# Kernel tuning notes

Hardware: AMD Instinct MI355X
Metric: run time of the kernel (lower is better)

The kernel has to match this reference:

```python
import jax, jax.numpy as jnp
import numpy as np

B_, T_, D_MODEL = 2, 2048, 1024
EXPAND, D_STATE, D_CONV, HEADDIM = 2, 128, 4, 64
D_INNER = EXPAND * D_MODEL            # 2048
NHEADS = D_INNER // HEADDIM           # 32
CONV_DIM = D_INNER + 2 * D_STATE      # 2304 (x, B, C share the depthwise conv)
D_IN_PROJ = 2 * D_INNER + 2 * D_STATE + NHEADS  # z, xBC, dt


def _rmsnorm(x, w, eps=1e-5):
    return x * jax.lax.rsqrt(jnp.mean(x * x, axis=-1, keepdims=True) + eps) * w


def setup_inputs() -> dict:
    key = jax.random.key(0)
    ks = jax.random.split(key, 8)
    def s(k, shape, scale=0.02):
        return jax.random.normal(k, shape, jnp.float32) * scale
    x = jax.random.normal(ks[0], (B_, T_, D_MODEL), jnp.float32)
    W_in = s(ks[1], (D_MODEL, D_IN_PROJ))
    conv_w = s(ks[2], (CONV_DIM, D_CONV), 0.1)
    conv_b = jnp.zeros((CONV_DIM,), jnp.float32)
    # dt_bias = softplus^-1(dt_init) with dt in [1e-3, 1e-1], per Mamba init
    dt0 = jax.random.uniform(ks[3], (NHEADS,), minval=1e-3, maxval=1e-1)
    dt_bias = jnp.log(jnp.expm1(dt0))
    A_log = jnp.log(jax.random.uniform(ks[4], (NHEADS,), minval=1.0, maxval=16.0))
    D = jnp.ones((NHEADS,), jnp.float32)
    norm_w = jnp.ones((D_MODEL,), jnp.float32)
    gnorm_w = jnp.ones((D_INNER,), jnp.float32)
    W_out = s(ks[5], (D_INNER, D_MODEL))
    return {"x": x, "W_in": W_in, "conv_w": conv_w, "conv_b": conv_b,
            "dt_bias": dt_bias, "A_log": A_log, "D": D,
            "norm_w": norm_w, "gnorm_w": gnorm_w, "W_out": W_out}


def reference(x, W_in, conv_w, conv_b, dt_bias, A_log, D, norm_w, gnorm_w, W_out):
    res = x
    xn = _rmsnorm(x, norm_w)                       # pre-norm
    zxbcdt = xn @ W_in                             # (B,T,D_IN_PROJ)
    z = zxbcdt[..., :D_INNER]
    xBC = zxbcdt[..., D_INNER:D_INNER + CONV_DIM]
    dt = zxbcdt[..., D_INNER + CONV_DIM:]          # (B,T,H)
    # causal depthwise conv over time on concat(x,B,C)
    inp = jnp.transpose(xBC, (0, 2, 1))            # (B,C,T)
    kern = conv_w[:, None, :]                      # (C,1,K)
    conv = jax.lax.conv_general_dilated(
        inp, kern, window_strides=(1,), padding=[(D_CONV - 1, 0)],
        feature_group_count=CONV_DIM, dimension_numbers=("NCH", "OIH", "NCH"))
    xBC = jax.nn.silu(jnp.transpose(conv, (0, 2, 1)) + conv_b)
    xs = xBC[..., :D_INNER].reshape(B_, T_, NHEADS, HEADDIM)  # (B,T,H,P)
    Bm = xBC[..., D_INNER:D_INNER + D_STATE]       # (B,T,N), ngroups=1
    C = xBC[..., D_INNER + D_STATE:]               # (B,T,N)
    dt = jax.nn.softplus(dt + dt_bias)             # (B,T,H)
    A = -jnp.exp(A_log)                            # (H,)

    def step(h, inps):
        x_t, B_t, C_t, dt_t = inps                 # (B,H,P),(B,N),(B,N),(B,H)
        da = jnp.exp(dt_t * A)                     # (B,H)
        h = h * da[:, :, None, None] + (dt_t[..., None] * x_t)[..., None] * B_t[:, None, None, :]
        y = jnp.einsum("bhpn,bn->bhp", h, C_t) + D[None, :, None] * x_t
        return h, y

    h0 = jnp.zeros((B_, NHEADS, HEADDIM, D_STATE), x.dtype)
    seq = (jnp.moveaxis(xs, 1, 0), jnp.moveaxis(Bm, 1, 0),
           jnp.moveaxis(C, 1, 0), jnp.moveaxis(dt, 1, 0))
    _, ys = jax.lax.scan(step, h0, seq)            # ys: (T,B,H,P)
    y = jnp.moveaxis(ys, 0, 1).reshape(B_, T_, D_INNER)
    y = _rmsnorm(y * jax.nn.silu(z), gnorm_w)      # gated RMSNorm
    return y @ W_out + res
```

## Files before the change

### kernel.cpp

```cpp
#include <hip/hip_runtime.h>
#include <hip/hip_bf16.h>

typedef unsigned short u16;
typedef unsigned int u32;
typedef u16 u16x8 __attribute__((ext_vector_type(8)));
typedef u16 u16x4 __attribute__((ext_vector_type(4)));
typedef __bf16 bf16x8 __attribute__((ext_vector_type(8)));
typedef float f32x4 __attribute__((ext_vector_type(4)));

#define B_SZ 2
#define T_SZ 2048
#define DMODEL 1024
#define DINNER 2048
#define DSTATE 128
#define NHEADS 32
#define HEADDIM 64
#define CONVDIM 2304
#define DINPROJ 4384
#define DINPROJ_P 4480
#define NROWS (B_SZ * T_SZ)
#define L_CH 128
#define NCH 16

__device__ __forceinline__ float bf2f(u16 u) {
    union { float f; u32 i; } v; v.i = ((u32)u) << 16; return v.f;
}
__device__ __forceinline__ u16 f2bf(float f) {
    union { float f; u32 i; } v; v.f = f;
    u32 r = v.i + 0x7FFFu + ((v.i >> 16) & 1u);
    return (u16)(r >> 16);
}
__device__ __forceinline__ bf16x8 ldfrag(const u16* p) {
    return __builtin_bit_cast(bf16x8, *(const u16x8*)p);
}
__device__ __forceinline__ void gload_lds16(const u16* g, u16* l) {
    __builtin_amdgcn_global_load_lds(
        (const __attribute__((address_space(1))) unsigned int*)g,
        (__attribute__((address_space(3))) unsigned int*)l, 16, 0, 0);
}

__device__ void trans_tile(const float* __restrict__ in, u16* __restrict__ out,
                           int K, int N, int n0, int k0)
{
    __shared__ u16 tile[64][72];
    const int tid = threadIdx.x;
#pragma unroll
    for (int r = 0; r < 4; r++) {
        int idx = r * 256 + tid;
        int k = idx >> 4, n4 = (idx & 15) << 2;
        const float* src = &in[(size_t)(k0 + k) * N + n0 + n4];
        float4 v;
        if (n0 + n4 + 3 < N) {
            v = *(const float4*)src;
        } else {
            v.x = (n0 + n4 + 0 < N) ? src[0] : 0.f;
            v.y = (n0 + n4 + 1 < N) ? src[1] : 0.f;
            v.z = (n0 + n4 + 2 < N) ? src[2] : 0.f;
            v.w = (n0 + n4 + 3 < N) ? src[3] : 0.f;
        }
        tile[n4 + 0][k] = f2bf(v.x);
        tile[n4 + 1][k] = f2bf(v.y);
        tile[n4 + 2][k] = f2bf(v.z);
        tile[n4 + 3][k] = f2bf(v.w);
    }
    __syncthreads();
#pragma unroll
    for (int r = 0; r < 2; r++) {
        int idx = r * 256 + tid;
        int n = idx >> 3, k8 = (idx & 7) << 3;
        u16x8 vv = *(const u16x8*)&tile[n][k8];
        *(u16x8*)&out[(size_t)(n0 + n) * K + k0 + k8] = vv;
    }
}

__global__ __launch_bounds__(256) void prep_kernel(
    const float* __restrict__ W_in, u16* __restrict__ W_inT,
    const float* __restrict__ W_out, u16* __restrict__ W_outT,
    const float* __restrict__ x, const float* __restrict__ nw, u16* __restrict__ xn,
    const float* __restrict__ cw, u16* __restrict__ cwT)
{
    const int blk = blockIdx.x;
    const int tid = threadIdx.x;
    if (blk < 1120) {
        trans_tile(W_in, W_inT, DMODEL, DINPROJ, (blk % 70) * 64, (blk / 70) * 64);
    } else if (blk < 1632) {
        int idx = blk - 1120;
        trans_tile(W_out, W_outT, DINNER, DMODEL, (idx % 16) * 64, (idx / 16) * 64);
    } else if (blk < 5728) {
        const int row = blk - 1632;
        float4 v = ((const float4*)(x + (size_t)row * DMODEL))[tid];
        float ss = v.x * v.x + v.y * v.y + v.z * v.z + v.w * v.w;
#pragma unroll
        for (int o = 32; o; o >>= 1) ss += __shfl_xor(ss, o);
        __shared__ float red[4];
        if ((tid & 63) == 0) red[tid >> 6] = ss;
        __syncthreads();
        ss = red[0] + red[1] + red[2] + red[3];
        float sc = rsqrtf(ss / (float)DMODEL + 1e-5f);
        float4 wv = ((const float4*)nw)[tid];
        u16x4 o4;
        o4[0] = f2bf(v.x * sc * wv.x);
        o4[1] = f2bf(v.y * sc * wv.y);
        o4[2] = f2bf(v.z * sc * wv.z);
        o4[3] = f2bf(v.w * sc * wv.w);
        *(u16x4*)&xn[(size_t)row * DMODEL + tid * 4] = o4;
    } else {
        for (int idx = tid; idx < 4 * CONVDIM; idx += 256) {
            int k = idx / CONVDIM, c = idx - k * CONVDIM;
            cwT[idx] = f2bf(cw[c * 4 + k]);
        }
    }
}

template<int MODE, int KC, int SWZ>
__global__ __launch_bounds__(256) void gemm128_kernel(
    const u16* __restrict__ A, const u16* __restrict__ BT, void* __restrict__ Cv,
    const float* __restrict__ Res, int Nst, int nbx)
{
    __shared__ u16 As[128 * 64];
    __shared__ u16 Bs[128 * 64];
    const int tid = threadIdx.x;
    const int l = tid & 63, w = tid >> 6;
    int m0, n0;
    if (SWZ) {
        const int bid = blockIdx.x;
        int s = (bid & 7) * 140 + (bid >> 3);
        int mc = s / 280, r2 = s - mc * 280;
        int nc = (r2 >= 144) ? 1 : 0;
        int local = r2 - nc * 144;
        int nloc = local >> 3, mloc = local & 7;
        m0 = (mc * 8 + mloc) * 128;
        n0 = (nc * 18 + nloc) * 128;
    } else {
        const int per = nbx * 8;
        const int grp = blockIdx.x / per, r = blockIdx.x % per;
        m0 = (grp * 8 + (r & 7)) * 128;
        n0 = (r >> 3) * 128;
    }
    const int ml = l & 15, quad = l >> 4;
    const int wm = (w & 1) * 64, wn = (w >> 1) * 64;
    f32x4 acc[4][4] = {};
    const int srow = l >> 3;
    const int sgx = (l & 7) ^ srow;
    const u16* Ag = A + (size_t)(m0 + w * 8 + srow) * KC + sgx * 8;
    const u16* Bg = BT + (size_t)(n0 + w * 8 + srow) * KC + sgx * 8;
    u16* const As_w = &As[(w * 8) * 64];
    u16* const Bs_w = &Bs[(w * 8) * 64];

#pragma unroll 4
    for (int k0 = 0; k0 < KC; k0 += 64) {
        __syncthreads();
#pragma unroll
        for (int j = 0; j < 4; j++) {
            gload_lds16(Ag + (size_t)(j * 32) * KC + k0, As_w + j * 32 * 64);
            gload_lds16(Bg + (size_t)(j * 32) * KC + k0, Bs_w + j * 32 * 64);
        }
        __syncthreads();
#pragma unroll
        for (int ks4 = 0; ks4 < 2; ks4++) {
            bf16x8 af[4], bfr[4];
#pragma unroll
            for (int i = 0; i < 4; i++)
                af[i] = ldfrag(&As[(wm + i * 16 + ml) * 64 +
                                   (((ks4 * 4 + quad) ^ (ml & 7)) * 8)]);
#pragma unroll
            for (int i = 0; i < 4; i++)
                bfr[i] = ldfrag(&Bs[(wn + i * 16 + ml) * 64 +
                                    (((ks4 * 4 + quad) ^ (ml & 7)) * 8)]);
#pragma unroll
            for (int mt = 0; mt < 4; mt++)
#pragma unroll
                for (int nt = 0; nt < 4; nt++)
                    acc[mt][nt] = __builtin_amdgcn_mfma_f32_16x16x32_bf16(
                        af[mt], bfr[nt], acc[mt][nt], 0, 0, 0);
        }
    }
#pragma unroll
    for (int mt = 0; mt < 4; mt++)
#pragma unroll
        for (int nt = 0; nt < 4; nt++)
#pragma unroll
            for (int rg = 0; rg < 4; rg++) {
                int m = m0 + wm + mt * 16 + quad * 4 + rg;
                int n = n0 + wn + nt * 16 + ml;
                if (n < Nst) {
                    if (MODE == 0)
                        ((u16*)Cv)[(size_t)m * Nst + n] = f2bf(acc[mt][nt][rg]);
                    else
                        ((float*)Cv)[(size_t)m * Nst + n] =
                            acc[mt][nt][rg] + Res[(size_t)m * Nst + n];
                }
            }
}

template<int KC>
__global__ __launch_bounds__(256) void gemm128x64_kernel(
    const u16* __restrict__ A, const u16* __restrict__ BT, float* __restrict__ C,
    const float* __restrict__ Res, int Nst)
{
    __shared__ u16 As[128 * 64];
    __shared__ u16 Bs[64 * 64];
    const int tid = threadIdx.x;
    const int l = tid & 63, w = tid >> 6;
    const int bid = blockIdx.x;
    const int xcd = bid & 7, local = bid >> 3;
    const int mc = xcd >> 1, nc = xcd & 1;
    const int nloc = local & 7, mloc = local >> 3;
    const int m0 = (mc * 8 + mloc) * 128;
    const int n0 = (nc * 8 + nloc) * 64;
    const int ml = l & 15, quad = l >> 4;
    const int wm = w * 32;
    f32x4 acc[2][4] = {};
    const int srow = l >> 3;
    const int sgx = (l & 7) ^ srow;
    const u16* Ag = A + (size_t)(m0 + w * 8 + srow) * KC + sgx * 8;
    const u16* Bg = BT + (size_t)(n0 + w * 8 + srow) * KC + sgx * 8;
    u16* const As_w = &As[(w * 8) * 64];
    u16* const Bs_w = &Bs[(w * 8) * 64];

#pragma unroll 4
    for (int k0 = 0; k0 < KC; k0 += 64) {
        __syncthreads();
#pragma unroll
        for (int j = 0; j < 4; j++)
            gload_lds16(Ag + (size_t)(j * 32) * KC + k0, As_w + j * 32 * 64);
#pragma unroll
        for (int j = 0; j < 2; j++)
            gload_lds16(Bg + (size_t)(j * 32) * KC + k0, Bs_w + j * 32 * 64);
        __syncthreads();
#pragma unroll
        for (int ks4 = 0; ks4 < 2; ks4++) {
            bf16x8 af[2], bfr[4];
#pragma unroll
            for (int i = 0; i < 2; i++)
                af[i] = ldfrag(&As[(wm + i * 16 + ml) * 64 +
                                   (((ks4 * 4 + quad) ^ (ml & 7)) * 8)]);
#pragma unroll
            for (int i = 0; i < 4; i++)
                bfr[i] = ldfrag(&Bs[(i * 16 + ml) * 64 +
                                    (((ks4 * 4 + quad) ^ (ml & 7)) * 8)]);
#pragma unroll
            for (int mt = 0; mt < 2; mt++)
#pragma unroll
                for (int nt = 0; nt < 4; nt++)
                    acc[mt][nt] = __builtin_amdgcn_mfma_f32_16x16x32_bf16(
                        bfr[nt], af[mt], acc[mt][nt], 0, 0, 0);
        }
    }
#pragma unroll
    for (int mt = 0; mt < 2; mt++) {
        const int m = m0 + wm + mt * 16 + ml;
#pragma unroll
        for (int nt = 0; nt < 4; nt++) {
            const int nb = n0 + nt * 16 + quad * 4;
            float4 r = *(const float4*)&Res[(size_t)m * Nst + nb];
            float4 o;
            o.x = acc[mt][nt][0] + r.x;
            o.y = acc[mt][nt][1] + r.y;
            o.z = acc[mt][nt][2] + r.z;
            o.w = acc[mt][nt][3] + r.w;
            *(float4*)&C[(size_t)m * Nst + nb] = o;
        }
    }
}

#define NGRAN (CONVDIM / 8)
__global__ __launch_bounds__(256) void conv_silu_kernel(
    const u16* __restrict__ zx, const u16* __restrict__ cwT,
    const float* __restrict__ cb, const float* __restrict__ dt_bias,
    u16* __restrict__ out, float* __restrict__ dts)
{
    int idx = blockIdx.x * 256 + threadIdx.x;
    if (idx < B_SZ * NHEADS * T_SZ) {
        int t = idx & (T_SZ - 1);
        int bh = idx >> 11;
        int h = bh & 31, b = bh >> 5;
        float v = bf2f(zx[(size_t)(b * T_SZ + t) * DINPROJ + (DINNER + CONVDIM) + h]) + dt_bias[h];
        float sp = (v > 20.f) ? v : log1pf(expf(v));
        dts[((size_t)bh << 11) + t] = sp;
    }
    int gr = idx % NGRAN;
    int bt = idx / NGRAN;
    int t = bt & (T_SZ - 1);
    int c0 = gr * 8;
    float acc[8];
#pragma unroll
    for (int u = 0; u < 8; u++) acc[u] = cb[c0 + u];
    const u16* base = zx + (size_t)bt * DINPROJ + DINNER + c0;
#pragma unroll
    for (int k = 0; k < 4; k++) {
        int tt = t - 3 + k;
        if (tt >= 0) {
            u16x8 xv = *(const u16x8*)(base + (ptrdiff_t)(k - 3) * DINPROJ);
            u16x8 wv = *(const u16x8*)&cwT[k * CONVDIM + c0];
#pragma unroll
            for (int u = 0; u < 8; u++)
                acc[u] += bf2f(xv[u]) * bf2f(wv[u]);
        }
    }
    u16 res[8];
#pragma unroll
    for (int u = 0; u < 8; u++) {
        float s = acc[u] / (1.f + expf(-acc[u]));
        res[u] = f2bf(s);
    }
    *(u16x8*)&out[(size_t)bt * CONVDIM + c0] = *(u16x8*)res;
}

__global__ __launch_bounds__(256) void chunk_state_kernel(
    const u16* __restrict__ xbc, const float* __restrict__ dts_g,
    const float* __restrict__ A_log, float* __restrict__ cs_g, u16* __restrict__ S_bf)
{
    const int g = blockIdx.x;
    const int b = g >> 9, rem = g & 511, c = rem >> 5, h = rem & 31;
    const int tid = threadIdx.x;
    __shared__ float tmp[128], dt_l[128], d2e[128];
    __shared__ u16 Xw[64][136];
    __shared__ u16 BsT[128][136];
    const float A = -__expf(A_log[h]);
    if (tid < 128) {
        float d = dts_g[(((size_t)(b * 32 + h)) << 11) + (c << 7) + tid];
        dt_l[tid] = d; tmp[tid] = d * A;
    }
    __syncthreads();
    for (int off = 1; off < 128; off <<= 1) {
        float add = 0.f;
        if (tid < 128 && tid >= off) add = tmp[tid - off];
        __syncthreads();
        if (tid < 128) tmp[tid] += add;
        __syncthreads();
    }
    if (tid < 128) {
        float cs = tmp[tid];
        cs_g[(((size_t)(b * 32 + h)) << 11) + (c << 7) + tid] = cs;
        d2e[tid] = __expf(tmp[127] - cs) * dt_l[tid];
    }
    __syncthreads();
    const size_t rowbase = ((size_t)(b * T_SZ + c * L_CH)) * CONVDIM;
#pragma unroll
    for (int r = 0; r < 4; r++) {
        int v = tid + r * 256;
        int t = v >> 3, p0 = (v & 7) << 3;
        u16x8 xv = *(const u16x8*)&xbc[rowbase + (size_t)t * CONVDIM + h * 64 + p0];
        float s = d2e[t];
        const int tc = (t & 7) | (((t >> 3) ^ ((p0 >> 3) & 15)) << 3);
#pragma unroll
        for (int u = 0; u < 8; u++) Xw[p0 + u][tc] = f2bf(bf2f(xv[u]) * s);
    }
#pragma unroll
    for (int r = 0; r < 8; r++) {
        int v = tid + r * 256;
        int t = v >> 4, n0 = (v & 15) << 3;
        u16x8 bv = *(const u16x8*)&xbc[rowbase + (size_t)t * CONVDIM + DINNER + n0];
        const int tc = (t & 7) | (((t >> 3) ^ ((n0 >> 3) & 15)) << 3);
#pragma unroll
        for (int u = 0; u < 8; u++) BsT[n0 + u][tc] = bv[u];
    }
    __syncthreads();
    const int lane = tid & 63, wv = tid >> 6, ml = lane & 15, quad = lane >> 4;
    f32x4 acc[8] = {};
    const int arow = wv * 16 + ml;
    const int asw = (arow >> 3) & 15;
    for (int k0 = 0; k0 < 128; k0 += 32) {
        bf16x8 af = ldfrag(&Xw[arow][(((k0 >> 3) + quad) ^ asw) << 3]);
#pragma unroll
        for (int nt = 0; nt < 8; nt++) {
            const int brow = nt * 16 + ml;
            bf16x8 bf = ldfrag(&BsT[brow][(((k0 >> 3) + quad) ^ ((brow >> 3) & 15)) << 3]);
            acc[nt] = __builtin_amdgcn_mfma_f32_16x16x32_bf16(bf, af, acc[nt], 0, 0, 0);
        }
    }
    const size_t base = (size_t)g * 8192;
    const int p = wv * 16 + ml;
#pragma unroll
    for (int nt = 0; nt < 8; nt++) {
        const int nb = nt * 16 + quad * 4;
        u16x4 pk;
#pragma unroll
        for (int rg = 0; rg < 4; rg++) pk[rg] = f2bf(acc[nt][rg]);
        *(u16x4*)&S_bf[base + p * 128 + nb] = pk;
    }
}

__global__ __launch_bounds__(256) void state_pass_kernel(
    const float* __restrict__ cs_g, u16* __restrict__ S_bf)
{
    const int bh = blockIdx.x >> 3, b = bh >> 5, h = bh & 31;
    const int off = (blockIdx.x & 7) * 1024 + threadIdx.x * 4;
    const float* csb = cs_g + (((size_t)(b * 32 + h)) << 11);
    float H[4] = {0.f, 0.f, 0.f, 0.f};
    const size_t step = (size_t)32 * 8192;
    size_t slot = ((size_t)(b * NCH * 32 + h)) * 8192 + off;
    u16x4 tv = *(const u16x4*)&S_bf[slot];
    for (int c = 0; c < NCH; c++) {
        u16x4 tvn = tv;
        if (c + 1 < NCH) tvn = *(const u16x4*)&S_bf[slot + step];
        float decay = __expf(csb[(c << 7) + 127]);
        u16x4 hw;
#pragma unroll
        for (int i = 0; i < 4; i++) hw[i] = f2bf(H[i]);
        *(u16x4*)&S_bf[slot] = hw;
#pragma unroll
        for (int i = 0; i < 4; i++) H[i] = H[i] * decay + bf2f(tv[i]);
        tv = tvn; slot += step;
    }
}

__global__ __launch_bounds__(256) void chunk_out_kernel(
    const u16* __restrict__ xbc, const float* __restrict__ dts_g,
    const float* __restrict__ cs_g, const u16* __restrict__ H_bf,
    const float* __restrict__ Dv, u16* __restrict__ yraw)
{
    const int g = blockIdx.x;
    const int b = g >> 9, rem = g & 511, c = rem >> 5, h = rem & 31;
    const int tid = threadIdx.x;
    __shared__ u16 Xs[64][136];
    __shared__ u16 Gs[128][40];
    __shared__ u16 Hs[64 * 128];
    __shared__ u16 Bsh[128 * 128];
    __shared__ float cs_l[128], P_l[128], dt_l[128];
    const size_t rowbase = ((size_t)(b * T_SZ + c * L_CH)) * CONVDIM;
    const u16* Cg = xbc + rowbase + DINNER + 128;
    const u16* Bg = xbc + rowbase + DINNER;
    const u16* Hg = H_bf + (size_t)g * 8192;
#pragma unroll
    for (int r = 0; r < 4; r++) {
        int i = r * 256 + tid;
        int row = i >> 4, slot = i & 15;
        gload_lds16(Hg + row * 128 + ((slot ^ (row & 15)) << 3), &Hs[i * 8]);
    }
#pragma unroll
    for (int r = 0; r < 8; r++) {
        int i = r * 256 + tid;
        int row = i >> 4, slot = i & 15;
        gload_lds16(Bg + (size_t)row * CONVDIM + ((slot ^ (row & 15)) << 3), &Bsh[i * 8]);
    }
    if (tid < 128) {
        float cs = cs_g[(((size_t)(b * 32 + h)) << 11) + (c << 7) + tid];
        cs_l[tid] = cs; P_l[tid] = __expf(cs);
        dt_l[tid] = dts_g[(((size_t)(b * 32 + h)) << 11) + (c << 7) + tid];
    }
#pragma unroll
    for (int r = 0; r < 4; r++) {
        int v = tid + r * 256; int t = v >> 3, p0 = (v & 7) << 3;
        u16x8 xv = *(const u16x8*)&xbc[rowbase + (size_t)t * CONVDIM + h * 64 + p0];
        const int tc = (t & 7) | (((t >> 3) ^ ((p0 >> 3) & 15)) << 3);
#pragma unroll
        for (int u = 0; u < 8; u++) Xs[p0 + u][tc] = xv[u];
    }
    __syncthreads();
    const int lane = tid & 63, wv = tid >> 6, ml = lane & 15, quad = lane >> 4;
    const int trow = wv * 32;
    bf16x8 cf[2][4];
#pragma unroll
    for (int mt = 0; mt < 2; mt++)
#pragma unroll
        for (int kk = 0; kk < 4; kk++)
            cf[mt][kk] = ldfrag(Cg + (size_t)(trow + mt * 16 + ml) * CONVDIM + kk * 32 + quad * 8);
    f32x4 accY[2][4] = {};
#pragma unroll
    for (int kk = 0; kk < 4; kk++) {
        const int sw = (((kk << 2) + quad) ^ ml) << 3;
#pragma unroll
        for (int pt = 0; pt < 4; pt++) {
            bf16x8 bf = ldfrag(&Hs[(pt * 16 + ml) * 128 + sw]);
            accY[0][pt] = __builtin_amdgcn_mfma_f32_16x16x32_bf16(cf[0][kk], bf, accY[0][pt], 0, 0, 0);
            accY[1][pt] = __builtin_amdgcn_mfma_f32_16x16x32_bf16(cf[1][kk], bf, accY[1][pt], 0, 0, 0);
        }
    }
#pragma unroll
    for (int mt = 0; mt < 2; mt++) {
#pragma unroll
        for (int rg = 0; rg < 4; rg++) {
            float pp = P_l[trow + mt * 16 + quad * 4 + rg];
#pragma unroll
            for (int pt = 0; pt < 4; pt++) accY[mt][pt][rg] *= pp;
        }
    }
    for (int js = 0; js < 4; js++) {
        const int j0 = js * 32;
        f32x4 Ga[2][2] = {};
#pragma unroll
        for (int kk = 0; kk < 4; kk++) {
            const int sw = (((kk << 2) + quad) ^ ml) << 3;
            bf16x8 bf0 = ldfrag(&Bsh[(j0 + ml) * 128 + sw]);
            bf16x8 bf1 = ldfrag(&Bsh[(j0 + 16 + ml) * 128 + sw]);
            Ga[0][0] = __builtin_amdgcn_mfma_f32_16x16x32_bf16(cf[0][kk], bf0, Ga[0][0], 0, 0, 0);
            Ga[0][1] = __builtin_amdgcn_mfma_f32_16x16x32_bf16(cf[0][kk], bf1, Ga[0][1], 0, 0, 0);
            Ga[1][0] = __builtin_amdgcn_mfma_f32_16x16x32_bf16(cf[1][kk], bf0, Ga[1][0], 0, 0, 0);
            Ga[1][1] = __builtin_amdgcn_mfma_f32_16x16x32_bf16(cf[1][kk], bf1, Ga[1][1], 0, 0, 0);
        }
#pragma unroll
        for (int mt = 0; mt < 2; mt++) {
#pragma unroll
            for (int jt = 0; jt < 2; jt++) {
#pragma unroll
                for (int rg = 0; rg < 4; rg++) {
                    int t = trow + mt * 16 + quad * 4 + rg;
                    int j = j0 + jt * 16 + ml;
                    float val = 0.f;
                    if (t >= j) val = Ga[mt][jt][rg] * __expf(cs_l[t] - cs_l[j]) * dt_l[j];
                    Gs[t][jt * 16 + ml] = f2bf(val);
                }
            }
        }
#pragma unroll
        for (int mt = 0; mt < 2; mt++) {
            bf16x8 ag = ldfrag(&Gs[trow + mt * 16 + ml][quad * 8]);
#pragma unroll
            for (int pt = 0; pt < 4; pt++) {
                const int xrow = pt * 16 + ml;
                bf16x8 bx = ldfrag(&Xs[xrow][(((j0 >> 3) + quad) ^ ((xrow >> 3) & 15)) << 3]);
                accY[mt][pt] = __builtin_amdgcn_mfma_f32_16x16x32_bf16(ag, bx, accY[mt][pt], 0, 0, 0);
            }
        }
    }
    const float Dh = Dv[h];
    const size_t ybase = ((size_t)(b * T_SZ + c * L_CH)) * DINNER;
#pragma unroll
    for (int mt = 0; mt < 2; mt++) {
#pragma unroll
        for (int pt = 0; pt < 4; pt++) {
#pragma unroll
            for (int rg = 0; rg < 4; rg++) {
                int t = trow + mt * 16 + quad * 4 + rg;
                int p = pt * 16 + ml;
                const int tc = (t & 7) | (((t >> 3) ^ ((p >> 3) & 15)) << 3);
                float v = accY[mt][pt][rg] + Dh * bf2f(Xs[p][tc]);
                yraw[ybase + (size_t)t * DINNER + h * 64 + p] = f2bf(v);
            }
        }
    }
}

__global__ __launch_bounds__(256) void postnorm_kernel(
    const u16* __restrict__ yraw, const u16* __restrict__ zx,
    const float* __restrict__ gw, u16* __restrict__ out)
{
    const int row = blockIdx.x;
    const int tid = threadIdx.x;
    u16x8 yv = *(const u16x8*)(yraw + (size_t)row * DINNER + tid * 8);
    u16x8 zv = *(const u16x8*)(zx + (size_t)row * DINPROJ + tid * 8);
    float vals[8]; float ss = 0.f;
#pragma unroll
    for (int i = 0; i < 8; i++) {
        float y = bf2f(yv[i]);
        float z = bf2f(zv[i]);
        float s = z / (1.f + expf(-z));
        float t = y * s; vals[i] = t; ss += t * t;
    }
#pragma unroll
    for (int o = 32; o; o >>= 1) ss += __shfl_xor(ss, o);
    __shared__ float red[4];
    if ((tid & 63) == 0) red[tid >> 6] = ss;
    __syncthreads();
    ss = red[0] + red[1] + red[2] + red[3];
    float sc = rsqrtf(ss / (float)DINNER + 1e-5f);
    u16 o8[8];
#pragma unroll
    for (int i = 0; i < 8; i++) o8[i] = f2bf(vals[i] * sc * gw[tid * 8 + i]);
    *(u16x8*)(out + (size_t)row * DINNER + tid * 8) = *(u16x8*)o8;
}

extern "C" void kernel_launch(void* const* d_in, const int* in_sizes, int n_in,
                              void* d_out, int out_size, void* d_ws, size_t ws_size,
                              hipStream_t stream) {
    const float* x       = (const float*)d_in[0];
    const float* W_in    = (const float*)d_in[1];
    const float* conv_w  = (const float*)d_in[2];
    const float* conv_b  = (const float*)d_in[3];
    const float* dt_bias = (const float*)d_in[4];
    const float* A_log   = (const float*)d_in[5];
    const float* Dv      = (const float*)d_in[6];
    const float* norm_w  = (const float*)d_in[7];
    const float* gnorm_w = (const float*)d_in[8];
    const float* W_out   = (const float*)d_in[9];
    float* out = (float*)d_out;

    char* ws = (char*)d_ws;
    u16*   xn    = (u16*)(ws);
    u16*   W_inT = (u16*)(ws + 8388608);
    u16*   S_bf  = (u16*)(ws);
    float* cs_g  = (float*)(ws + 16777216);
    u16*   zx    = (u16*)(ws + 17563648);
    u16*   xbc   = (u16*)(ws + 53477376);
    float* dts   = (float*)(ws + 72351744);
    u16*   yraw  = (u16*)(ws + 72876032);
    u16*   cwT   = (u16*)(ws + 89653248);
    u16*   W_outT= (u16*)(ws + 89671680);
    u16*   ynorm = yraw;

    prep_kernel<<<5729, 256, 0, stream>>>(
        W_in, W_inT, W_out, W_outT, x, norm_w, xn, conv_w, cwT);
    gemm128_kernel<0, DMODEL, 1><<<(DINPROJ_P / 128) * (NROWS / 128), 256, 0, stream>>>(
        xn, W_inT, zx, nullptr, DINPROJ, DINPROJ_P / 128);
    conv_silu_kernel<<<(NROWS * NGRAN) / 256, 256, 0, stream>>>(
        zx, cwT, conv_b, dt_bias, xbc, dts);
    chunk_state_kernel<<<B_SZ * NCH * NHEADS, 256, 0, stream>>>(xbc, dts, A_log, cs_g, S_bf);
    state_pass_kernel<<<B_SZ * NHEADS * 8, 256, 0, stream>>>(cs_g, S_bf);
    chunk_out_kernel<<<B_SZ * NCH * NHEADS, 256, 0, stream>>>(xbc, dts, cs_g, S_bf, Dv, yraw);
    postnorm_kernel<<<NROWS, 256, 0, stream>>>(yraw, zx, gnorm_w, ynorm);
    gemm128x64_kernel<DINNER><<<512, 256, 0, stream>>>(
        ynorm, W_outT, out, x, DMODEL);
}
```

Baseline: 261.1 us.

## Reuse conv input rows over 4 timesteps, shuffle scan, transpose MFMA outputs for packed stores

The conv+SiLU kernel now has each thread produce four consecutive timesteps. It loads 7 input rows and the 4 weight vectors once into registers instead of re-reading overlapping rows, and the launch grid is cut by four. The chunk_state prefix sum over dt*A uses a wavefront __shfl_up scan plus one cross-wave add, replacing the log-step shared-memory scan and its many barriers. In chunk_out the MFMA A/B operands are swapped so each lane owns a timestep row. That lets the G-matrix and y outputs be written as packed 4-element stores instead of scattered 2-byte stores. The new conv path uses more registers and has a redundant load-guard block.

```diff
diff --git a/kernel.cpp b/kernel.cpp
--- a/kernel.cpp
+++ b/kernel.cpp
@@ -280,31 +280,48 @@
         dts[((size_t)bh << 11) + t] = sp;
     }
     int gr = idx % NGRAN;
-    int bt = idx / NGRAN;
-    int t = bt & (T_SZ - 1);
+    int q  = idx / NGRAN;
+    int bt0 = q * 4;
+    int t0 = bt0 & (T_SZ - 1);
     int c0 = gr * 8;
-    float acc[8];
-#pragma unroll
-    for (int u = 0; u < 8; u++) acc[u] = cb[c0 + u];
-    const u16* base = zx + (size_t)bt * DINPROJ + DINNER + c0;
-#pragma unroll
-    for (int k = 0; k < 4; k++) {
-        int tt = t - 3 + k;
-        if (tt >= 0) {
-            u16x8 xv = *(const u16x8*)(base + (ptrdiff_t)(k - 3) * DINPROJ);
-            u16x8 wv = *(const u16x8*)&cwT[k * CONVDIM + c0];
+    const u16* base = zx + (size_t)bt0 * DINPROJ + DINNER + c0;
+    u16x8 xr[7];
+#pragma unroll
+    for (int i = 0; i < 7; i++) {
+        int tt = t0 + i - 3;
+        if (tt >= 0 && i < 7 - 0) {
+            xr[i] = (tt >= 0) ? *(const u16x8*)(base + (ptrdiff_t)(i - 3) * DINPROJ)
+                              : u16x8{};
+        }
+        if (tt < 0) xr[i] = u16x8{};
+        else xr[i] = *(const u16x8*)(base + (ptrdiff_t)(i - 3) * DINPROJ);
+    }
+    u16x8 wv[4];
+#pragma unroll
+    for (int k = 0; k < 4; k++) wv[k] = *(const u16x8*)&cwT[k * CONVDIM + c0];
+    float bias[8];
+#pragma unroll
+    for (int u = 0; u < 8; u++) bias[u] = cb[c0 + u];
+#pragma unroll
+    for (int u4 = 0; u4 < 4; u4++) {
+        float acc[8];
+#pragma unroll
+        for (int u = 0; u < 8; u++) acc[u] = bias[u];
+#pragma unroll
+        for (int k = 0; k < 4; k++) {
+            u16x8 xv = xr[u4 + k];
 #pragma unroll
             for (int u = 0; u < 8; u++)
-                acc[u] += bf2f(xv[u]) * bf2f(wv[u]);
-        }
-    }
-    u16 res[8];
-#pragma unroll
-    for (int u = 0; u < 8; u++) {
-        float s = acc[u] / (1.f + expf(-acc[u]));
-        res[u] = f2bf(s);
-    }
-    *(u16x8*)&out[(size_t)bt * CONVDIM + c0] = *(u16x8*)res;
+                acc[u] += bf2f(xv[u]) * bf2f(wv[k][u]);
+        }
+        u16 res[8];
+#pragma unroll
+        for (int u = 0; u < 8; u++) {
+            float s = acc[u] / (1.f + expf(-acc[u]));
+            res[u] = f2bf(s);
+        }
+        *(u16x8*)&out[(size_t)(bt0 + u4) * CONVDIM + c0] = *(u16x8*)res;
+    }
 }
 
 __global__ __launch_bounds__(256) void chunk_state_kernel(
@@ -315,32 +332,38 @@
     const int b = g >> 9, rem = g & 511, c = rem >> 5, h = rem & 31;
     const int tid = threadIdx.x;
     __shared__ float tmp[128], dt_l[128], d2e[128];
+    __shared__ float wtot;
     __shared__ u16 Xw[64][136];
     __shared__ u16 BsT[128][136];
     const float A = -__expf(A_log[h]);
+    float v = 0.f;
     if (tid < 128) {
         float d = dts_g[(((size_t)(b * 32 + h)) << 11) + (c << 7) + tid];
-        dt_l[tid] = d; tmp[tid] = d * A;
+        dt_l[tid] = d;
+        v = d * A;
+#pragma unroll
+        for (int off = 1; off < 64; off <<= 1) {
+            float pv = __shfl_up(v, off, 64);
+            if ((tid & 63) >= off) v += pv;
+        }
+        if (tid == 63) wtot = v;
     }
     __syncthreads();
-    for (int off = 1; off < 128; off <<= 1) {
-        float add = 0.f;
-        if (tid < 128 && tid >= off) add = tmp[tid - off];
-        __syncthreads();
-        if (tid < 128) tmp[tid] += add;
-        __syncthreads();
-    }
     if (tid < 128) {
-        float cs = tmp[tid];
-        cs_g[(((size_t)(b * 32 + h)) << 11) + (c << 7) + tid] = cs;
-        d2e[tid] = __expf(tmp[127] - cs) * dt_l[tid];
+        if (tid >= 64) v += wtot;
+        tmp[tid] = v;
+        cs_g[(((size_t)(b * 32 + h)) << 11) + (c << 7) + tid] = v;
+    }
+    __syncthreads();
+    if (tid < 128) {
+        d2e[tid] = __expf(tmp[127] - v) * dt_l[tid];
     }
     __syncthreads();
     const size_t rowbase = ((size_t)(b * T_SZ + c * L_CH)) * CONVDIM;
 #pragma unroll
     for (int r = 0; r < 4; r++) {
-        int v = tid + r * 256;
-        int t = v >> 3, p0 = (v & 7) << 3;
+        int vv = tid + r * 256;
+        int t = vv >> 3, p0 = (vv & 7) << 3;
         u16x8 xv = *(const u16x8*)&xbc[rowbase + (size_t)t * CONVDIM + h * 64 + p0];
         float s = d2e[t];
         const int tc = (t & 7) | (((t >> 3) ^ ((p0 >> 3) & 15)) << 3);
@@ -349,8 +372,8 @@
     }
 #pragma unroll
     for (int r = 0; r < 8; r++) {
-        int v = tid + r * 256;
-        int t = v >> 4, n0 = (v & 15) << 3;
+        int vv = tid + r * 256;
+        int t = vv >> 4, n0 = (vv & 15) << 3;
         u16x8 bv = *(const u16x8*)&xbc[rowbase + (size_t)t * CONVDIM + DINNER + n0];
         const int tc = (t & 7) | (((t >> 3) ^ ((n0 >> 3) & 15)) << 3);
 #pragma unroll
@@ -464,18 +487,17 @@
 #pragma unroll
         for (int pt = 0; pt < 4; pt++) {
             bf16x8 bf = ldfrag(&Hs[(pt * 16 + ml) * 128 + sw]);
-            accY[0][pt] = __builtin_amdgcn_mfma_f32_16x16x32_bf16(cf[0][kk], bf, accY[0][pt], 0, 0, 0);
-            accY[1][pt] = __builtin_amdgcn_mfma_f32_16x16x32_bf16(cf[1][kk], bf, accY[1][pt], 0, 0, 0);
+            accY[0][pt] = __builtin_amdgcn_mfma_f32_16x16x32_bf16(bf, cf[0][kk], accY[0][pt], 0, 0, 0);
+            accY[1][pt] = __builtin_amdgcn_mfma_f32_16x16x32_bf16(bf, cf[1][kk], accY[1][pt], 0, 0, 0);
         }
     }
 #pragma unroll
     for (int mt = 0; mt < 2; mt++) {
-#pragma unroll
-        for (int rg = 0; rg < 4; rg++) {
-            float pp = P_l[trow + mt * 16 + quad * 4 + rg];
-#pragma unroll
-            for (int pt = 0; pt < 4; pt++) accY[mt][pt][rg] *= pp;
-        }
+        const float pp = P_l[trow + mt * 16 + ml];
+#pragma unroll
+        for (int pt = 0; pt < 4; pt++)
+#pragma unroll
+            for (int rg = 0; rg < 4; rg++) accY[mt][pt][rg] *= pp;
     }
     for (int js = 0; js < 4; js++) {
         const int j0 = js * 32;
@@ -485,23 +507,26 @@
             const int sw = (((kk << 2) + quad) ^ ml) << 3;
             bf16x8 bf0 = ldfrag(&Bsh[(j0 + ml) * 128 + sw]);
             bf16x8 bf1 = ldfrag(&Bsh[(j0 + 16 + ml) * 128 + sw]);
-            Ga[0][0] = __builtin_amdgcn_mfma_f32_16x16x32_bf16(cf[0][kk], bf0, Ga[0][0], 0, 0, 0);
-            Ga[0][1] = __builtin_amdgcn_mfma_f32_16x16x32_bf16(cf[0][kk], bf1, Ga[0][1], 0, 0, 0);
-            Ga[1][0] = __builtin_amdgcn_mfma_f32_16x16x32_bf16(cf[1][kk], bf0, Ga[1][0], 0, 0, 0);
-            Ga[1][1] = __builtin_amdgcn_mfma_f32_16x16x32_bf16(cf[1][kk], bf1, Ga[1][1], 0, 0, 0);
+            Ga[0][0] = __builtin_amdgcn_mfma_f32_16x16x32_bf16(bf0, cf[0][kk], Ga[0][0], 0, 0, 0);
+            Ga[0][1] = __builtin_amdgcn_mfma_f32_16x16x32_bf16(bf1, cf[0][kk], Ga[0][1], 0, 0, 0);
+            Ga[1][0] = __builtin_amdgcn_mfma_f32_16x16x32_bf16(bf0, cf[1][kk], Ga[1][0], 0, 0, 0);
+            Ga[1][1] = __builtin_amdgcn_mfma_f32_16x16x32_bf16(bf1, cf[1][kk], Ga[1][1], 0, 0, 0);
         }
 #pragma unroll
         for (int mt = 0; mt < 2; mt++) {
+            const int t = trow + mt * 16 + ml;
+            const float cst = cs_l[t];
 #pragma unroll
             for (int jt = 0; jt < 2; jt++) {
+                u16x4 pk;
 #pragma unroll
                 for (int rg = 0; rg < 4; rg++) {
-                    int t = trow + mt * 16 + quad * 4 + rg;
-                    int j = j0 + jt * 16 + ml;
+                    int j = j0 + jt * 16 + quad * 4 + rg;
                     float val = 0.f;
-                    if (t >= j) val = Ga[mt][jt][rg] * __expf(cs_l[t] - cs_l[j]) * dt_l[j];
-                    Gs[t][jt * 16 + ml] = f2bf(val);
+                    if (t >= j) val = Ga[mt][jt][rg] * __expf(cst - cs_l[j]) * dt_l[j];
+                    pk[rg] = f2bf(val);
                 }
+                *(u16x4*)&Gs[t][jt * 16 + quad * 4] = pk;
             }
         }
 #pragma unroll
@@ -511,7 +536,7 @@
             for (int pt = 0; pt < 4; pt++) {
                 const int xrow = pt * 16 + ml;
                 bf16x8 bx = ldfrag(&Xs[xrow][(((j0 >> 3) + quad) ^ ((xrow >> 3) & 15)) << 3]);
-                accY[mt][pt] = __builtin_amdgcn_mfma_f32_16x16x32_bf16(ag, bx, accY[mt][pt], 0, 0, 0);
+                accY[mt][pt] = __builtin_amdgcn_mfma_f32_16x16x32_bf16(bx, ag, accY[mt][pt], 0, 0, 0);
             }
         }
     }
@@ -519,16 +544,16 @@
     const size_t ybase = ((size_t)(b * T_SZ + c * L_CH)) * DINNER;
 #pragma unroll
     for (int mt = 0; mt < 2; mt++) {
+        const int t = trow + mt * 16 + ml;
 #pragma unroll
         for (int pt = 0; pt < 4; pt++) {
-#pragma unroll
-            for (int rg = 0; rg < 4; rg++) {
-                int t = trow + mt * 16 + quad * 4 + rg;
-                int p = pt * 16 + ml;
-                const int tc = (t & 7) | (((t >> 3) ^ ((p >> 3) & 15)) << 3);
-                float v = accY[mt][pt][rg] + Dh * bf2f(Xs[p][tc]);
-                yraw[ybase + (size_t)t * DINNER + h * 64 + p] = f2bf(v);
-            }
+            const int pb = pt * 16 + quad * 4;
+            const int tc = (t & 7) | (((t >> 3) ^ ((pb >> 3) & 15)) << 3);
+            u16x4 pk;
+#pragma unroll
+            for (int rg = 0; rg < 4; rg++)
+                pk[rg] = f2bf(accY[mt][pt][rg] + Dh * bf2f(Xs[pb + rg][tc]));
+            *(u16x4*)&yraw[ybase + (size_t)t * DINNER + h * 64 + pb] = pk;
         }
     }
 }
@@ -594,7 +619,7 @@
         W_in, W_inT, W_out, W_outT, x, norm_w, xn, conv_w, cwT);
     gemm128_kernel<0, DMODEL, 1><<<(DINPROJ_P / 128) * (NROWS / 128), 256, 0, stream>>>(
         xn, W_inT, zx, nullptr, DINPROJ, DINPROJ_P / 128);
-    conv_silu_kernel<<<(NROWS * NGRAN) / 256, 256, 0, stream>>>(
+    conv_silu_kernel<<<(NROWS / 4 * NGRAN) / 256, 256, 0, stream>>>(
         zx, cwT, conv_b, dt_bias, xbc, dts);
     chunk_state_kernel<<<B_SZ * NCH * NHEADS, 256, 0, stream>>>(xbc, dts, A_log, cs_g, S_bf);
     state_pass_kernel<<<B_SZ * NHEADS * 8, 256, 0, stream>>>(cs_g, S_bf);
```

After: 254.3 us. 2.6% less time.
